# Performance work log

Hardware: AMD Instinct MI355X
Metric: run time of the kernel (lower is better)

The kernel has to match this reference:

```python
import jax, jax.numpy as jnp
import numpy as np

S, B, F, H, L = 256, 64, 512, 512, 4
INV_SQRT_H = float(1.0 / np.sqrt(H))


def _ln(x, g, b, eps=1e-5):
    # torch nn.LayerNorm: biased variance, eps=1e-5
    mu = jnp.mean(x, axis=-1, keepdims=True)
    var = jnp.var(x, axis=-1, keepdims=True)
    return (x - mu) * jax.lax.rsqrt(var + eps) * g + b


def setup_inputs() -> dict:
    key = jax.random.key(0)
    k1, k2 = jax.random.split(key)
    x = jax.random.normal(k1, (S, B, F), dtype=jnp.float32)  # time-major [S,B,F]
    W = jax.random.normal(k2, (L, 6, F, H), dtype=jnp.float32) * 0.02  # q,k,v,i,f,o
    b = jnp.zeros((L, 6, H), jnp.float32)
    ln_g = jnp.ones((L, 6, H), jnp.float32)
    ln_b = jnp.zeros((L, 6, H), jnp.float32)
    return {"x": x, "W": W, "b": b, "ln_g": ln_g, "ln_b": ln_b}


def reference(x, W, b, ln_g, ln_b):
    # Dropout is identity (eval mode / p effectively 0).
    def step(carry, x_t):
        h, c, n = carry  # each [L,B,H]
        layer_input = x_t  # [B,F]
        hs, cs, ns = [], [], []
        for l in range(L):
            # all 6 gate projections in one einsum: [6,B,H]
            z = jnp.einsum('bf,gfh->gbh', layer_input, W[l]) + b[l][:, None, :]
            z = z.at[1].multiply(INV_SQRT_H)  # k = Wk(x)/sqrt(H) before LN
            z = _ln(z, ln_g[l][:, None, :], ln_b[l][:, None, :])
            q, k, v = z[0], z[1], z[2]
            i = jax.nn.sigmoid(z[3])
            f = jax.nn.sigmoid(z[4])
            o = jax.nn.sigmoid(z[5])
            # (k[:,:,None] @ v[:,None,:]).sum(dim=1) == k.sum(-1,keepdims)*v
            kv_sum = jnp.sum(k, axis=-1, keepdims=True) * v
            c_l = f * c[l] + i * kv_sum
            n_l = f * n[l] + i * k
            n_hat = n_l / (jnp.linalg.norm(n_l, axis=-1, keepdims=True) + 1e-8)
            h_l = o * jnp.tanh(q * n_hat)
            if l > 0:  # residual_conn
                h_l = h_l + layer_input
            layer_input = h_l
            hs.append(h_l); cs.append(c_l); ns.append(n_l)
        h = jnp.stack(hs); c = jnp.stack(cs); n = jnp.stack(ns)
        return (h, c, n), h[-1]

    init = tuple(jnp.zeros((L, B, H), x.dtype) for _ in range(3))
    (h, c, n), out = jax.lax.scan(step, init, x)  # out: [S,B,H] time-major
    return out, h, c, n
```

## Files before the change

### kernel.cpp

```cpp
#include <hip/hip_runtime.h>


typedef unsigned short u16;
typedef unsigned int   u32;
typedef short s8v  __attribute__((ext_vector_type(8)));
typedef float f16v __attribute__((ext_vector_type(16)));

#define S_    256
#define B_    64
#define F_    512
#define H_    512
#define L_    4
#define NG    3072
#define RALL  16384
#define CH    16
#define INV_SQRT_H 0.044194173824159216f

__device__ __forceinline__ float bu2f(u16 u) {
    union { u32 i; float f; } z; z.i = ((u32)u) << 16; return z.f;
}
__device__ __forceinline__ u16 f2bf(float f) {
    union { float f; u32 i; } z; z.f = f;
    u32 r = (z.i + 0x7FFFu + ((z.i >> 16) & 1u)) >> 16;
    return (u16)r;
}
__device__ __forceinline__ float sigm(float x)  { return 1.0f / (1.0f + __expf(-x)); }
__device__ __forceinline__ float tanhf_(float x){ return 2.0f / (1.0f + __expf(-2.0f * x)) - 1.0f; }
__device__ __forceinline__ float wred64(float v) {
    #pragma unroll
    for (int m = 1; m < 64; m <<= 1) v += __shfl_xor(v, m);
    return v;
}
__device__ __forceinline__ void gl_lds16(const u16* g, u16* l) {
    __builtin_amdgcn_global_load_lds((const __attribute__((address_space(1))) u32*)g,
                                     (__attribute__((address_space(3))) u32*)l, 16, 0, 0);
}
__device__ __forceinline__ void unp8(uint4 u, float* f) {
    f[0] = bu2f((u16)(u.x & 0xffff)); f[1] = bu2f((u16)(u.x >> 16));
    f[2] = bu2f((u16)(u.y & 0xffff)); f[3] = bu2f((u16)(u.y >> 16));
    f[4] = bu2f((u16)(u.z & 0xffff)); f[5] = bu2f((u16)(u.z >> 16));
    f[6] = bu2f((u16)(u.w & 0xffff)); f[7] = bu2f((u16)(u.w >> 16));
}
__device__ __forceinline__ uint4 pck8(const float* f) {
    uint4 u;
    u.x = (u32)f2bf(f[0]) | ((u32)f2bf(f[1]) << 16);
    u.y = (u32)f2bf(f[2]) | ((u32)f2bf(f[3]) << 16);
    u.z = (u32)f2bf(f[4]) | ((u32)f2bf(f[5]) << 16);
    u.w = (u32)f2bf(f[6]) | ((u32)f2bf(f[7]) << 16);
    return u;
}

__global__ void convw_k(const float* __restrict__ W, u16* __restrict__ WT) {
    __shared__ float tile[32][33];
    const int lg = blockIdx.z;
    const int h0 = blockIdx.x * 32, f0 = blockIdx.y * 32;
    const float* Wb = W  + (size_t)lg * F_ * H_;
    u16*        WTb = WT + (size_t)lg * F_ * H_;
    const int tx = threadIdx.x, ty = threadIdx.y;
    #pragma unroll
    for (int i = 0; i < 32; i += 8)
        tile[ty + i][tx] = Wb[(size_t)(f0 + ty + i) * H_ + h0 + tx];
    __syncthreads();
    #pragma unroll
    for (int i = 0; i < 32; i += 8)
        WTb[(size_t)(h0 + ty + i) * F_ + f0 + tx] = f2bf(tile[tx][ty + i]);
}

__global__ void convx_k(const float* __restrict__ x, u16* __restrict__ A) {
    const int i = blockIdx.x * 256 + threadIdx.x;
    float4 v = ((const float4*)x)[i];
    u32 lo = (u32)f2bf(v.x) | ((u32)f2bf(v.y) << 16);
    u32 hi = (u32)f2bf(v.z) | ((u32)f2bf(v.w) << 16);
    ((uint2*)A)[i] = make_uint2(lo, hi);
}

__global__ __launch_bounds__(256) void gemm_k(const u16* __restrict__ A,
                                              const u16* __restrict__ BT,
                                              u16* __restrict__ Z,
                                              const float* __restrict__ bias,
                                              int arow0) {
    __shared__ u16 lsA[128 * 64];
    __shared__ u16 lsB[128 * 64];
    const int t = threadIdx.x;
    const int ntile = blockIdx.x;
    const int mtile = blockIdx.y;
    const int ncol0 = ntile * 128;
    const u16* Ab = A  + (size_t)(arow0 + mtile * 128) * F_;
    const u16* Bb = BT + (size_t)ntile * 128 * F_;
    const int lane = t & 63, wv = t >> 6;

    f16v acc[2][2];
    #pragma unroll
    for (int i = 0; i < 2; i++)
        #pragma unroll
        for (int j = 0; j < 2; j++) acc[i][j] = 0.0f;

    const int wm = (wv >> 1) * 64, wn = (wv & 1) * 64;
    const int rl = lane & 31, hi = lane >> 5;
    const int r7 = rl & 7;

    int goff[4];
    #pragma unroll
    for (int s = 0; s < 4; s++) {
        const int c = t + 256 * s;
        const int row = c >> 3, slot = c & 7;
        const int g = slot ^ (row & 7);
        goff[s] = row * F_ + g * 8;
    }

    for (int kb = 0; kb < 8; ++kb) {
        const int kofs = kb * 64;
        #pragma unroll
        for (int s = 0; s < 4; s++) {
            const int c = t + 256 * s;
            gl_lds16(Ab + goff[s] + kofs, lsA + c * 8);
            gl_lds16(Bb + goff[s] + kofs, lsB + c * 8);
        }
        __syncthreads();
        #pragma unroll
        for (int s = 0; s < 4; ++s) {
            const int slot = ((s << 1) + hi) ^ r7;
            s8v fa[2], fb[2];
            #pragma unroll
            for (int i = 0; i < 2; i++)
                fa[i] = *(const s8v*)(lsA + (wm + i * 32 + rl) * 64 + slot * 8);
            #pragma unroll
            for (int j = 0; j < 2; j++)
                fb[j] = *(const s8v*)(lsB + (wn + j * 32 + rl) * 64 + slot * 8);
            #pragma unroll
            for (int i = 0; i < 2; i++)
                #pragma unroll
                for (int j = 0; j < 2; j++)
                    acc[i][j] = __builtin_amdgcn_mfma_f32_32x32x16_bf16(fa[i], fb[j], acc[i][j], 0, 0, 0);
        }
        __syncthreads();
    }

    #pragma unroll
    for (int j = 0; j < 2; j++) {
        const int col = ncol0 + wn + j * 32 + rl;
        const float bv = bias[col];
        #pragma unroll
        for (int i = 0; i < 2; i++) {
            const int mbase = mtile * 128 + wm + i * 32 + hi * 4;
            #pragma unroll
            for (int reg = 0; reg < 16; reg++) {
                const int row = mbase + (reg & 3) + 8 * (reg >> 2);
                Z[(size_t)row * NG + col] = f2bf(acc[i][j][reg] + bv);
            }
        }
    }
}

__global__ __launch_bounds__(256) void stats_k(const u16* __restrict__ Z,
                                               const float* __restrict__ lng1,
                                               const float* __restrict__ lnb1,
                                               float* __restrict__ stats) {
    const int wid = threadIdx.x >> 6, lane = threadIdx.x & 63;
    const int row = blockIdx.x * 4 + wid;
    const u16* zr = Z + (size_t)row * NG + lane * 8;

    float g1v[8], b1v[8];
    #pragma unroll
    for (int j = 0; j < 8; j++) { g1v[j] = lng1[lane * 8 + j]; b1v[j] = lnb1[lane * 8 + j]; }

    float s[4], sq[4], wk = 0.f, sg1 = 0.f, sb1 = 0.f;
    #pragma unroll
    for (int g = 0; g < 4; ++g) {
        uint4 u = *(const uint4*)(zr + (g + 1) * 512);
        float f[8];
        unp8(u, f);
        float ls = 0.f, lq = 0.f;
        #pragma unroll
        for (int j = 0; j < 8; j++) { ls += f[j]; lq += f[j] * f[j]; }
        s[g] = ls; sq[g] = lq;
        if (g == 0) {
            #pragma unroll
            for (int j = 0; j < 8; j++) wk += g1v[j] * f[j];
        }
    }
    #pragma unroll
    for (int j = 0; j < 8; j++) { sg1 += g1v[j]; sb1 += b1v[j]; }

    #pragma unroll
    for (int g = 0; g < 4; ++g) { s[g] = wred64(s[g]); sq[g] = wred64(sq[g]); }
    wk = wred64(wk); sg1 = wred64(sg1); sb1 = wred64(sb1);

    if (lane == 0) {
        float* o = stats + (size_t)row * 16;
        const float inv = 1.0f / 512.0f;
        float mu1 = 0.f, rs1 = 0.f;
        #pragma unroll
        for (int g = 0; g < 4; ++g) {
            float m = s[g] * inv, e2 = sq[g] * inv;
            if (g == 0) { m *= INV_SQRT_H; e2 *= INV_SQRT_H * INV_SQRT_H; }
            const float rs = rsqrtf(fmaxf(e2 - m * m, 0.0f) + 1e-5f);
            o[1 + g] = m; o[7 + g] = rs;
            if (g == 0) { mu1 = m; rs1 = rs; }
        }
        o[12] = rs1 * (INV_SQRT_H * wk - mu1 * sg1) + sb1;
    }
}

__global__ __launch_bounds__(128) void scanA_k(const u16* __restrict__ Z,
                                               const float* __restrict__ stats,
                                               const float* __restrict__ lngl,
                                               const float* __restrict__ lnbl,
                                               u16* __restrict__ nbuf,
                                               u16* __restrict__ pbuf,
                                               float* __restrict__ sumP,
                                               float* __restrict__ sumC,
                                               float* __restrict__ sumN) {
    const int b = blockIdx.y, chunk = blockIdx.z;
    const int h = blockIdx.x * 128 + threadIdx.x;
    __shared__ float sst[CH][16];
    for (int i = threadIdx.x; i < CH * 16; i += 128) {
        const int tc = i >> 4, j = i & 15;
        sst[tc][j] = stats[(size_t)((chunk * CH + tc) * 64 + b) * 16 + j];
    }
    float gg[4], gb[4];
    #pragma unroll
    for (int g = 0; g < 4; ++g) {
        gg[g] = lngl[(g + 1) * 512 + h];
        gb[g] = lnbl[(g + 1) * 512 + h];
    }
    __syncthreads();

    float c = 0.f, n = 0.f, P = 1.f;
    #pragma unroll 4
    for (int tc = 0; tc < CH; ++tc) {
        const int r = (chunk * CH + tc) * 64 + b;
        const u16* zr = Z + (size_t)r * NG + h;
        const float z1 = bu2f(zr[512]);
        const float z2 = bu2f(zr[1024]);
        const float z3 = bu2f(zr[1536]);
        const float z4 = bu2f(zr[2048]);
        const float kk = (z1 * INV_SQRT_H - sst[tc][1]) * sst[tc][7] * gg[0] + gb[0];
        const float vv = (z2 - sst[tc][2]) * sst[tc][8]  * gg[1] + gb[1];
        const float ii = sigm((z3 - sst[tc][3]) * sst[tc][9]  * gg[2] + gb[2]);
        const float ff = sigm((z4 - sst[tc][4]) * sst[tc][10] * gg[3] + gb[3]);
        c = ff * c + ii * (sst[tc][12] * vv);
        n = ff * n + ii * kk;
        P *= ff;
        nbuf[(size_t)r * 512 + h] = f2bf(n);
        pbuf[(size_t)r * 512 + h] = f2bf(P);
    }
    const size_t idx = ((size_t)chunk << 15) + (b << 9) + h;
    sumP[idx] = P; sumC[idx] = c; sumN[idx] = n;
}

__global__ __launch_bounds__(256) void scanB_k(const float* __restrict__ sumP,
                                               const float* __restrict__ sumC,
                                               const float* __restrict__ sumN,
                                               float* __restrict__ n0buf,
                                               float* __restrict__ cstate,
                                               float* __restrict__ nstate,
                                               float* __restrict__ finals,
                                               int t0, int NC, int l) {
    const int idx = blockIdx.x * 256 + threadIdx.x;
    float c, n;
    if (t0 == 0) { c = 0.f; n = 0.f; }
    else { c = cstate[idx]; n = nstate[idx]; }
    for (int ch = 0; ch < NC; ++ch) {
        const size_t o = ((size_t)ch << 15) + idx;
        n0buf[o] = n;
        const float P = sumP[o];
        c = sumC[o] + P * c;
        n = sumN[o] + P * n;
    }
    if (t0 + NC * CH == S_) {
        const int b = idx >> 9, h = idx & 511;
        const size_t so = ((size_t)l * B_ + b) * H_ + h;
        finals[(size_t)L_ * B_ * H_ + so] = c;
        finals[(size_t)2 * L_ * B_ * H_ + so] = n;
    } else {
        cstate[idx] = c; nstate[idx] = n;
    }
}

__global__ __launch_bounds__(256) void normh_k(const u16* __restrict__ Z,
                                               const u16* __restrict__ nbuf,
                                               const u16* __restrict__ pbuf,
                                               const float* __restrict__ n0buf,
                                               const float* __restrict__ lngl,
                                               const float* __restrict__ lnbl,
                                               float* __restrict__ hbuf,
                                               u16* __restrict__ aoutB,
                                               float* __restrict__ outp,
                                               float* __restrict__ finals,
                                               int t0, int l) {
    const int wid = threadIdx.x >> 6, lane = threadIdx.x & 63;
    const int r = blockIdx.x * 4 + wid;
    const int h0 = lane * 8;

    float nl[8], pv[8];
    unp8(*(const uint4*)(nbuf + (size_t)r * 512 + h0), nl);
    unp8(*(const uint4*)(pbuf + (size_t)r * 512 + h0), pv);
    const float* n0r = n0buf + ((size_t)(r >> 10) << 15) + ((size_t)(r & 63) << 9) + h0;
    const float4 na = *(const float4*)(n0r);
    const float4 nb = *(const float4*)(n0r + 4);
    const float n0v[8] = {na.x, na.y, na.z, na.w, nb.x, nb.y, nb.z, nb.w};

    const u16* zr = Z + (size_t)r * NG;
    float z0[8], z5[8];
    unp8(*(const uint4*)(zr + h0), z0);
    unp8(*(const uint4*)(zr + 2560 + h0), z5);

    float nsq = 0.f, s0 = 0.f, q0 = 0.f, s5 = 0.f, q5 = 0.f;
    float nv[8];
    #pragma unroll
    for (int j = 0; j < 8; j++) {
        nv[j] = fmaf(pv[j], n0v[j], nl[j]);
        nsq += nv[j] * nv[j];
        s0 += z0[j]; q0 += z0[j] * z0[j];
        s5 += z5[j]; q5 += z5[j] * z5[j];
    }
    nsq = wred64(nsq);
    s0 = wred64(s0); q0 = wred64(q0);
    s5 = wred64(s5); q5 = wred64(q5);
    const float rinv = 1.0f / (sqrtf(nsq) + 1e-8f);
    const float inv = 1.0f / 512.0f;
    const float mu0 = s0 * inv, mu5 = s5 * inv;
    const float rs0 = rsqrtf(fmaxf(q0 * inv - mu0 * mu0, 0.0f) + 1e-5f);
    const float rs5 = rsqrtf(fmaxf(q5 * inv - mu5 * mu5, 0.0f) + 1e-5f);

    float g0[8], b0[8], g5[8], b5[8];
    #pragma unroll
    for (int j = 0; j < 8; j++) {
        g0[j] = lngl[h0 + j];        b0[j] = lnbl[h0 + j];
        g5[j] = lngl[2560 + h0 + j]; b5[j] = lnbl[2560 + h0 + j];
    }

    const int tl = r >> 6, b = r & 63;
    const int gr = t0 + tl;
    const size_t grow = (((size_t)gr * 64 + b) * 512) + h0;

    float hv[8];
    #pragma unroll
    for (int j = 0; j < 8; j++) {
        const float q  = (z0[j] - mu0) * rs0 * g0[j] + b0[j];
        const float oo = sigm((z5[j] - mu5) * rs5 * g5[j] + b5[j]);
        hv[j] = oo * tanhf_(q * nv[j] * rinv);
    }
    if (l > 0) {
        #pragma unroll
        for (int j = 0; j < 8; j++) hv[j] += hbuf[grow + j];
    }
    if (outp) {
        #pragma unroll
        for (int j = 0; j < 8; j++) outp[grow + j] = hv[j];
    } else {
        #pragma unroll
        for (int j = 0; j < 8; j++) hbuf[grow + j] = hv[j];
    }
    if (aoutB) *(uint4*)(aoutB + grow) = pck8(hv);

    if (gr == S_ - 1) {
        const size_t so = (((size_t)l * B_ + b) * 512) + h0;
        #pragma unroll
        for (int j = 0; j < 8; j++) finals[so + j] = hv[j];
    }
}

extern "C" void kernel_launch(void* const* d_in, const int* in_sizes, int n_in,
                              void* d_out, int out_size, void* d_ws, size_t ws_size,
                              hipStream_t stream) {
    const float* x   = (const float*)d_in[0];
    const float* W   = (const float*)d_in[1];
    const float* bia = (const float*)d_in[2];
    const float* lng = (const float*)d_in[3];
    const float* lnb = (const float*)d_in[4];
    float* out = (float*)d_out;

    const size_t WT_B = (size_t)L_ * 6 * H_ * F_ * 2;
    const size_t A_B  = (size_t)RALL * F_ * 2;
    const size_t ST_B = (size_t)RALL * 16 * 4;
    const size_t CS_B = (size_t)B_ * H_ * 4;
    const size_t HB_B = (size_t)RALL * H_ * 4;
    auto zB  = [](int T) { return (size_t)T * B_ * NG * 2; };
    auto nB  = [](int T) { return (size_t)T * B_ * H_ * 2; };
    auto cxB = [](int T) { return (size_t)(T / CH) * B_ * H_ * 4; };
    const size_t base = WT_B + A_B + ST_B + 2 * CS_B + HB_B + 32768;

    int T = 16;
    const int cand[3] = {256, 64, 16};
    for (int i = 0; i < 3; i++) {
        const int Tc = cand[i];
        if (ws_size >= base + zB(Tc) + 2 * nB(Tc) + 4 * cxB(Tc)) { T = Tc; break; }
    }
    const int NC = T / CH;

    char* ws = (char*)d_ws;
    size_t off = 0;
    auto take = [&](size_t nb) { size_t o = off; off += (nb + 255) & ~(size_t)255; return o; };
    u16*   WT    = (u16*)  (ws + take(WT_B));
    u16*   Abf   = (u16*)  (ws + take(A_B));
    float* stats = (float*)(ws + take(ST_B));
    float* cs    = (float*)(ws + take(CS_B));
    float* ns    = (float*)(ws + take(CS_B));
    float* hbuf  = (float*)(ws + take(HB_B));
    u16*   zb    = (u16*)  (ws + take(zB(T)));
    u16*   nbuf  = (u16*)  (ws + take(nB(T)));
    u16*   pbuf  = (u16*)  (ws + take(nB(T)));
    float* sumP  = (float*)(ws + take(cxB(T)));
    float* sumC  = (float*)(ws + take(cxB(T)));
    float* sumN  = (float*)(ws + take(cxB(T)));
    float* n0buf = (float*)(ws + take(cxB(T)));

    convw_k<<<dim3(16, 16, 24), dim3(32, 8), 0, stream>>>(W, WT);
    convx_k<<<dim3(RALL * F_ / 4 / 256), dim3(256), 0, stream>>>(x, Abf);

    float* finals = out + (size_t)S_ * B_ * H_;
    for (int l = 0; l < L_; ++l) {
        const u16*   WTl   = WT  + (size_t)l * 6 * H_ * F_;
        const float* biasl = bia + (size_t)l * NG;
        const float* lngl  = lng + (size_t)l * 6 * H_;
        const float* lnbl  = lnb + (size_t)l * 6 * H_;
        for (int j = 0; j < S_ / T; ++j) {
            const int t0 = j * T, arow0 = t0 * B_;
            const int rows = T * B_;
            gemm_k<<<dim3(24, rows / 128), dim3(256), 0, stream>>>(Abf, WTl, zb, biasl, arow0);
            stats_k<<<dim3(rows / 4), dim3(256), 0, stream>>>(zb, lngl + H_, lnbl + H_, stats);
            scanA_k<<<dim3(4, B_, NC), dim3(128), 0, stream>>>(zb, stats, lngl, lnbl,
                                                               nbuf, pbuf, sumP, sumC, sumN);
            scanB_k<<<dim3(128), dim3(256), 0, stream>>>(sumP, sumC, sumN, n0buf,
                                                         cs, ns, finals, t0, NC, l);
            normh_k<<<dim3(rows / 4), dim3(256), 0, stream>>>(zb, nbuf, pbuf, n0buf,
                                                              lngl, lnbl, hbuf,
                                                              (l < 3) ? Abf : (u16*)nullptr,
                                                              (l == 3) ? out : (float*)nullptr,
                                                              finals, t0, l);
        }
    }
}
```

Measured before the change: 605.9 us.

## Fuse LayerNorm stats into scan kernel, swizzle GEMM tiles, drop fp32 residual buffer

The separate stats kernel is folded into a new 512-thread scan kernel. Each block first loads its chunk's k/v/i/f gate rows into LDS, computes the per-row LayerNorm statistics with wave reductions, then runs the chunked recurrence reading from LDS instead of global memory. This removes a launch per step and a second global read of Z. The GEMM grid becomes 1D with a swizzle that groups consecutive tiles by blockIdx modulo 8, which likely targets locality per XCD. The fp32 hbuf residual buffer is removed: normh now reads the residual from and writes back into the bf16 activation buffer, which cuts memory traffic but lowers the precision of the residual path.

```diff
diff --git a/kernel.cpp b/kernel.cpp
--- a/kernel.cpp
+++ b/kernel.cpp
@@ -82,8 +82,11 @@
     __shared__ u16 lsA[128 * 64];
     __shared__ u16 lsB[128 * 64];
     const int t = threadIdx.x;
-    const int ntile = blockIdx.x;
-    const int mtile = blockIdx.y;
+
+    const int bid = blockIdx.x, nwg = gridDim.x;
+    const int cpx = nwg >> 3;
+    const int swz = (bid & 7) * cpx + (bid >> 3);
+    const int ntile = swz % 24, mtile = swz / 24;
     const int ncol0 = ntile * 128;
     const u16* Ab = A  + (size_t)(arow0 + mtile * 128) * F_;
     const u16* Bb = BT + (size_t)ntile * 128 * F_;
@@ -152,58 +155,7 @@
     }
 }
 
-__global__ __launch_bounds__(256) void stats_k(const u16* __restrict__ Z,
-                                               const float* __restrict__ lng1,
-                                               const float* __restrict__ lnb1,
-                                               float* __restrict__ stats) {
-    const int wid = threadIdx.x >> 6, lane = threadIdx.x & 63;
-    const int row = blockIdx.x * 4 + wid;
-    const u16* zr = Z + (size_t)row * NG + lane * 8;
-
-    float g1v[8], b1v[8];
-    #pragma unroll
-    for (int j = 0; j < 8; j++) { g1v[j] = lng1[lane * 8 + j]; b1v[j] = lnb1[lane * 8 + j]; }
-
-    float s[4], sq[4], wk = 0.f, sg1 = 0.f, sb1 = 0.f;
-    #pragma unroll
-    for (int g = 0; g < 4; ++g) {
-        uint4 u = *(const uint4*)(zr + (g + 1) * 512);
-        float f[8];
-        unp8(u, f);
-        float ls = 0.f, lq = 0.f;
-        #pragma unroll
-        for (int j = 0; j < 8; j++) { ls += f[j]; lq += f[j] * f[j]; }
-        s[g] = ls; sq[g] = lq;
-        if (g == 0) {
-            #pragma unroll
-            for (int j = 0; j < 8; j++) wk += g1v[j] * f[j];
-        }
-    }
-    #pragma unroll
-    for (int j = 0; j < 8; j++) { sg1 += g1v[j]; sb1 += b1v[j]; }
-
-    #pragma unroll
-    for (int g = 0; g < 4; ++g) { s[g] = wred64(s[g]); sq[g] = wred64(sq[g]); }
-    wk = wred64(wk); sg1 = wred64(sg1); sb1 = wred64(sb1);
-
-    if (lane == 0) {
-        float* o = stats + (size_t)row * 16;
-        const float inv = 1.0f / 512.0f;
-        float mu1 = 0.f, rs1 = 0.f;
-        #pragma unroll
-        for (int g = 0; g < 4; ++g) {
-            float m = s[g] * inv, e2 = sq[g] * inv;
-            if (g == 0) { m *= INV_SQRT_H; e2 *= INV_SQRT_H * INV_SQRT_H; }
-            const float rs = rsqrtf(fmaxf(e2 - m * m, 0.0f) + 1e-5f);
-            o[1 + g] = m; o[7 + g] = rs;
-            if (g == 0) { mu1 = m; rs1 = rs; }
-        }
-        o[12] = rs1 * (INV_SQRT_H * wk - mu1 * sg1) + sb1;
-    }
-}
-
-__global__ __launch_bounds__(128) void scanA_k(const u16* __restrict__ Z,
-                                               const float* __restrict__ stats,
+__global__ __launch_bounds__(512) void scans_k(const u16* __restrict__ Z,
                                                const float* __restrict__ lngl,
                                                const float* __restrict__ lnbl,
                                                u16* __restrict__ nbuf,
@@ -211,35 +163,80 @@
                                                float* __restrict__ sumP,
                                                float* __restrict__ sumC,
                                                float* __restrict__ sumN) {
-    const int b = blockIdx.y, chunk = blockIdx.z;
-    const int h = blockIdx.x * 128 + threadIdx.x;
-    __shared__ float sst[CH][16];
-    for (int i = threadIdx.x; i < CH * 16; i += 128) {
-        const int tc = i >> 4, j = i & 15;
-        sst[tc][j] = stats[(size_t)((chunk * CH + tc) * 64 + b) * 16 + j];
-    }
+    __shared__ u16  zs[CH][4][512];
+    __shared__ float st[CH][9];
+    const int b = blockIdx.x, chunk = blockIdx.y;
+    const int t = threadIdx.x;
+    const int wid = t >> 6, lane = t & 63;
+    const float inv = 1.0f / 512.0f;
+
+    float g1v[8], sg1 = 0.f, sb1 = 0.f;
+    #pragma unroll
+    for (int j = 0; j < 8; j++) {
+        g1v[j] = lngl[512 + lane * 8 + j];
+        sg1 += g1v[j];
+        sb1 += lnbl[512 + lane * 8 + j];
+    }
+    sg1 = wred64(sg1); sb1 = wred64(sb1);
+
+    #pragma unroll
+    for (int rr = 0; rr < 2; ++rr) {
+        const int tc = wid * 2 + rr;
+        const int row = (chunk * CH + tc) * 64 + b;
+        const u16* zr = Z + (size_t)row * NG + lane * 8;
+        float s[4], sq[4], wk = 0.f;
+        #pragma unroll
+        for (int g = 0; g < 4; ++g) {
+            uint4 u = *(const uint4*)(zr + (g + 1) * 512);
+            *(uint4*)&zs[tc][g][lane * 8] = u;
+            float f[8]; unp8(u, f);
+            float ls = 0.f, lq = 0.f;
+            #pragma unroll
+            for (int j = 0; j < 8; j++) { ls += f[j]; lq += f[j] * f[j]; }
+            s[g] = ls; sq[g] = lq;
+            if (g == 0) {
+                #pragma unroll
+                for (int j = 0; j < 8; j++) wk += g1v[j] * f[j];
+            }
+        }
+        #pragma unroll
+        for (int g = 0; g < 4; ++g) { s[g] = wred64(s[g]); sq[g] = wred64(sq[g]); }
+        wk = wred64(wk);
+        if (lane == 0) {
+            float mu1 = 0.f, rs1 = 0.f;
+            #pragma unroll
+            for (int g = 0; g < 4; ++g) {
+                float m = s[g] * inv, e2 = sq[g] * inv;
+                if (g == 0) { m *= INV_SQRT_H; e2 *= INV_SQRT_H * INV_SQRT_H; }
+                const float rs = rsqrtf(fmaxf(e2 - m * m, 0.0f) + 1e-5f);
+                st[tc][g] = m; st[tc][4 + g] = rs;
+                if (g == 0) { mu1 = m; rs1 = rs; }
+            }
+            st[tc][8] = rs1 * (INV_SQRT_H * wk - mu1 * sg1) + sb1;
+        }
+    }
+    __syncthreads();
+
+    const int h = t;
     float gg[4], gb[4];
     #pragma unroll
     for (int g = 0; g < 4; ++g) {
         gg[g] = lngl[(g + 1) * 512 + h];
         gb[g] = lnbl[(g + 1) * 512 + h];
     }
-    __syncthreads();
-
     float c = 0.f, n = 0.f, P = 1.f;
     #pragma unroll 4
     for (int tc = 0; tc < CH; ++tc) {
         const int r = (chunk * CH + tc) * 64 + b;
-        const u16* zr = Z + (size_t)r * NG + h;
-        const float z1 = bu2f(zr[512]);
-        const float z2 = bu2f(zr[1024]);
-        const float z3 = bu2f(zr[1536]);
-        const float z4 = bu2f(zr[2048]);
-        const float kk = (z1 * INV_SQRT_H - sst[tc][1]) * sst[tc][7] * gg[0] + gb[0];
-        const float vv = (z2 - sst[tc][2]) * sst[tc][8]  * gg[1] + gb[1];
-        const float ii = sigm((z3 - sst[tc][3]) * sst[tc][9]  * gg[2] + gb[2]);
-        const float ff = sigm((z4 - sst[tc][4]) * sst[tc][10] * gg[3] + gb[3]);
-        c = ff * c + ii * (sst[tc][12] * vv);
+        const float z1 = bu2f(zs[tc][0][h]);
+        const float z2 = bu2f(zs[tc][1][h]);
+        const float z3 = bu2f(zs[tc][2][h]);
+        const float z4 = bu2f(zs[tc][3][h]);
+        const float kk = (z1 * INV_SQRT_H - st[tc][0]) * st[tc][4] * gg[0] + gb[0];
+        const float vv = (z2 - st[tc][1]) * st[tc][5] * gg[1] + gb[1];
+        const float ii = sigm((z3 - st[tc][2]) * st[tc][6] * gg[2] + gb[2]);
+        const float ff = sigm((z4 - st[tc][3]) * st[tc][7] * gg[3] + gb[3]);
+        c = ff * c + ii * (st[tc][8] * vv);
         n = ff * n + ii * kk;
         P *= ff;
         nbuf[(size_t)r * 512 + h] = f2bf(n);
@@ -284,8 +281,7 @@
                                                const float* __restrict__ n0buf,
                                                const float* __restrict__ lngl,
                                                const float* __restrict__ lnbl,
-                                               float* __restrict__ hbuf,
-                                               u16* __restrict__ aoutB,
+                                               u16* abuf,
                                                float* __restrict__ outp,
                                                float* __restrict__ finals,
                                                int t0, int l) {
@@ -343,17 +339,17 @@
         hv[j] = oo * tanhf_(q * nv[j] * rinv);
     }
     if (l > 0) {
-        #pragma unroll
-        for (int j = 0; j < 8; j++) hv[j] += hbuf[grow + j];
+        float rv[8];
+        unp8(*(const uint4*)(abuf + grow), rv);
+        #pragma unroll
+        for (int j = 0; j < 8; j++) hv[j] += rv[j];
     }
     if (outp) {
         #pragma unroll
         for (int j = 0; j < 8; j++) outp[grow + j] = hv[j];
     } else {
-        #pragma unroll
-        for (int j = 0; j < 8; j++) hbuf[grow + j] = hv[j];
-    }
-    if (aoutB) *(uint4*)(aoutB + grow) = pck8(hv);
+        *(uint4*)(abuf + grow) = pck8(hv);
+    }
 
     if (gr == S_ - 1) {
         const size_t so = (((size_t)l * B_ + b) * 512) + h0;
@@ -374,13 +370,11 @@
 
     const size_t WT_B = (size_t)L_ * 6 * H_ * F_ * 2;
     const size_t A_B  = (size_t)RALL * F_ * 2;
-    const size_t ST_B = (size_t)RALL * 16 * 4;
     const size_t CS_B = (size_t)B_ * H_ * 4;
-    const size_t HB_B = (size_t)RALL * H_ * 4;
     auto zB  = [](int T) { return (size_t)T * B_ * NG * 2; };
     auto nB  = [](int T) { return (size_t)T * B_ * H_ * 2; };
     auto cxB = [](int T) { return (size_t)(T / CH) * B_ * H_ * 4; };
-    const size_t base = WT_B + A_B + ST_B + 2 * CS_B + HB_B + 32768;
+    const size_t base = WT_B + A_B + 2 * CS_B + 32768;
 
     int T = 16;
     const int cand[3] = {256, 64, 16};
@@ -395,10 +389,8 @@
     auto take = [&](size_t nb) { size_t o = off; off += (nb + 255) & ~(size_t)255; return o; };
     u16*   WT    = (u16*)  (ws + take(WT_B));
     u16*   Abf   = (u16*)  (ws + take(A_B));
-    float* stats = (float*)(ws + take(ST_B));
     float* cs    = (float*)(ws + take(CS_B));
     float* ns    = (float*)(ws + take(CS_B));
-    float* hbuf  = (float*)(ws + take(HB_B));
     u16*   zb    = (u16*)  (ws + take(zB(T)));
     u16*   nbuf  = (u16*)  (ws + take(nB(T)));
     u16*   pbuf  = (u16*)  (ws + take(nB(T)));
@@ -419,15 +411,13 @@
         for (int j = 0; j < S_ / T; ++j) {
             const int t0 = j * T, arow0 = t0 * B_;
             const int rows = T * B_;
-            gemm_k<<<dim3(24, rows / 128), dim3(256), 0, stream>>>(Abf, WTl, zb, biasl, arow0);
-            stats_k<<<dim3(rows / 4), dim3(256), 0, stream>>>(zb, lngl + H_, lnbl + H_, stats);
-            scanA_k<<<dim3(4, B_, NC), dim3(128), 0, stream>>>(zb, stats, lngl, lnbl,
-                                                               nbuf, pbuf, sumP, sumC, sumN);
+            gemm_k<<<dim3(24 * (rows / 128)), dim3(256), 0, stream>>>(Abf, WTl, zb, biasl, arow0);
+            scans_k<<<dim3(B_, NC), dim3(512), 0, stream>>>(zb, lngl, lnbl,
+                                                            nbuf, pbuf, sumP, sumC, sumN);
             scanB_k<<<dim3(128), dim3(256), 0, stream>>>(sumP, sumC, sumN, n0buf,
                                                          cs, ns, finals, t0, NC, l);
             normh_k<<<dim3(rows / 4), dim3(256), 0, stream>>>(zb, nbuf, pbuf, n0buf,
-                                                              lngl, lnbl, hbuf,
-                                                              (l < 3) ? Abf : (u16*)nullptr,
+                                                              lngl, lnbl, Abf,
                                                               (l == 3) ? out : (float*)nullptr,
                                                               finals, t0, l);
         }
```

New measurement: 589.3 us. -2.7%, faster.
